# Performance work log

Hardware: AMD Instinct MI355X
Metric: run time of the kernel (lower is better)

## Reference

```python
import jax, jax.numpy as jnp
import numpy as np
from jax import lax

B, C, H, L = 4, 64, 8, 2048  # batch, per-head channels, heads, sequence length


def setup_inputs() -> dict:
    key = jax.random.key(0)
    ks = jax.random.split(key, 15)

    def p(k, shape, s=0.05):
        return jax.random.normal(k, shape, jnp.float32) * s

    inp = {"x": jax.random.normal(ks[0], (B, C, L), jnp.float32)}
    for i, nm in enumerate(["q", "k", "v"]):
        inp[f"{nm}_dw"] = p(ks[1 + 4 * i], (C, 1, 3))       # depthwise conv weight, groups=C, k=3
        inp[f"{nm}_db"] = p(ks[2 + 4 * i], (C,))
        inp[f"{nm}_pw"] = p(ks[3 + 4 * i], (H * C, C))      # pointwise 1x1 conv weight
        inp[f"{nm}_pb"] = p(ks[4 + 4 * i], (H * C,))
    inp["u_w"] = p(ks[13], (C, H * C))                      # unify_heads 1x1 conv weight
    inp["u_b"] = p(ks[14], (C,))
    return inp


def dsconv(x, dw, db, pw, pb):
    # Depth-separable conv1d: depthwise (k=3, pad=1, groups=C) then pointwise 1x1.
    c = x.shape[1]
    y = lax.conv_general_dilated(x, dw, window_strides=(1,), padding=[(1, 1)],
                                 dimension_numbers=("NCH", "OIH", "NCH"),
                                 feature_group_count=c)
    y = y + db[None, :, None]
    return jnp.einsum("bcl,oc->bol", y, pw) + pb[None, :, None]


def reference(x, q_dw, q_db, q_pw, q_pb, k_dw, k_db, k_pw, k_pb,
              v_dw, v_db, v_pw, v_pb, u_w, u_b):
    b, c, l = x.shape
    h = H
    scale = c ** (-0.25)
    q = dsconv(x, q_dw, q_db, q_pw, q_pb).reshape(b, h, c, l) * scale
    k = dsconv(x, k_dw, k_db, k_pw, k_pb).reshape(b, h, c, l) * scale
    v = dsconv(x, v_dw, v_db, v_pw, v_pb).reshape(b, h, c, l)
    # dot[b,h,i,j] = sum_c k[b,h,c,i] * q[b,h,c,j]  (i = key pos, j = query pos)
    dot = jnp.einsum("bhci,bhcj->bhij", k, q)
    att = jax.nn.softmax(dot, axis=2)  # normalize over key positions (torch dim=1 of [bh,l,l])
    out = jnp.einsum("bhci,bhij->bhcj", v, att).reshape(b, h * c, l)
    return jnp.einsum("bkl,ck->bcl", out, u_w) + u_b[None, :, None]
```

## Files before the change

kernel.cpp:

```cpp
#include <hip/hip_runtime.h>
#include <hip/hip_bf16.h>
#include <stdint.h>
#include <string.h>

typedef unsigned short u16;
typedef unsigned int u32;
typedef __bf16 bf16x8 __attribute__((ext_vector_type(8)));
typedef float f32x4 __attribute__((ext_vector_type(4)));
typedef unsigned int u32x2v __attribute__((ext_vector_type(2)));

#define NB 4
#define NC 64
#define NH 8
#define NL 2048
#define HC 512

#define XT_OFF  ((size_t)0)
#define WM_OFF  ((size_t)1 << 20)
#define PBM_OFF ((size_t)2 << 20)
#define V_OFF   ((size_t)4 << 20)
#define QT_OFF  ((size_t)12 << 20)
#define KT_OFF  ((size_t)20 << 20)

#define LP 68

#if __has_builtin(__builtin_amdgcn_exp2f)
#define EXP2F __builtin_amdgcn_exp2f
#else
#define EXP2F exp2f
#endif

static __device__ __forceinline__ u16 f2bfu(float f) {
  union { float f; unsigned int i; } x; x.f = f;
  unsigned int i = x.i;
  return (u16)((i + 0x7fffu + ((i >> 16) & 1u)) >> 16);
}
static __device__ __forceinline__ u32 pk2(float a, float b) {
  float2 f; f.x = a; f.y = b;
  __hip_bfloat162 h = __float22bfloat162_rn(f);
  u32 w; __builtin_memcpy(&w, &h, 4); return w;
}
static __device__ __forceinline__ bf16x8 ld_bf8(const u16* p) {
  bf16x8 v; __builtin_memcpy(&v, p, 16); return v;
}
static __device__ __forceinline__ bf16x8 frag_from4(u32 a, u32 b, u32 c, u32 d) {
  u32 t[4] = {a, b, c, d};
  bf16x8 v; __builtin_memcpy(&v, t, 16); return v;
}
static __device__ __forceinline__ void st_frag(u16* p, u32 a, u32 b, u32 c, u32 d) {
  u32 t[4] = {a, b, c, d};
  __builtin_memcpy(p, t, 16);
}

#define XCHG(X_, Y_, Fa_, Fb_)                                              \
  {                                                                         \
    u32x2v a_ = __builtin_amdgcn_permlane32_swap((X_), (Y_), false, false); \
    u32x2v b_ = __builtin_amdgcn_permlane16_swap(a_.x, a_.y, false, false); \
    Fa_ = b_.x; Fb_ = b_.y;                                                 \
  }

__global__ __launch_bounds__(256) void prep_all(
    const float* __restrict__ x,
    const float* __restrict__ qdw, const float* __restrict__ qdb,
    const float* __restrict__ qpw, const float* __restrict__ qpb,
    const float* __restrict__ kdw, const float* __restrict__ kdb,
    const float* __restrict__ kpw, const float* __restrict__ kpb,
    const float* __restrict__ vdw, const float* __restrict__ vdb,
    const float* __restrict__ vpw, const float* __restrict__ vpb,
    const float* __restrict__ ub,
    u16* __restrict__ Wm, float* __restrict__ pbm,
    u16* __restrict__ xT, float* __restrict__ out)
{
  __shared__ __align__(16) u16 T[64 * LP];
  int bx = blockIdx.x;
  int tid = threadIdx.x;

  if (bx < 512) {
    int i4 = bx * 256 + tid;
    int c = (i4 >> 9) & 63;
    float f = ub[c];
    float4 v = {f, f, f, f};
    ((float4*)out)[i4] = v;
    return;
  }
  if (bx < 902) {
    int idx = (bx - 512) * 256 + tid;
    if (idx < 98304) {
      int tns = idx >> 15, r = idx & 32767, o = r >> 6, c = r & 63;
      const float* dw = (tns == 0) ? qdw : (tns == 1) ? kdw : vdw;
      const float* pw = (tns == 0) ? qpw : (tns == 1) ? kpw : vpw;
      float s = (tns == 0) ? 0.35355339059327373f * 1.4426950408889634f
              : (tns == 1) ? 0.35355339059327373f : 1.0f;
      float w = pw[o * 64 + c] * s;
#pragma unroll
      for (int d = 0; d < 3; ++d)
        Wm[((size_t)(tns * 3 + d) * 512 + o) * 64 + c] = f2bfu(w * dw[c * 3 + d]);
    } else {
      int i = idx - 98304;
      int tns = i >> 9, o = i & 511;
      const float* db = (tns == 0) ? qdb : (tns == 1) ? kdb : vdb;
      const float* pw = (tns == 0) ? qpw : (tns == 1) ? kpw : vpw;
      const float* pb = (tns == 0) ? qpb : (tns == 1) ? kpb : vpb;
      float s = (tns == 0) ? 0.35355339059327373f * 1.4426950408889634f
              : (tns == 1) ? 0.35355339059327373f : 1.0f;
      float bias = pb[o];
      for (int c = 0; c < 64; ++c) bias += pw[o * 64 + c] * db[c];
      pbm[i] = bias * s;
    }
    return;
  }
  {
    int b2 = bx - 902;
    int lt = b2 & 31, b = b2 >> 5;
    {
      int c = tid & 63, ls = (tid >> 6) * 16;
      const float4* g = (const float4*)(x + ((size_t)b * NC + c) * NL + lt * 64 + ls);
      u16 tmp[16];
#pragma unroll
      for (int j4 = 0; j4 < 4; ++j4) {
        float4 f = g[j4];
        tmp[j4*4+0] = f2bfu(f.x); tmp[j4*4+1] = f2bfu(f.y);
        tmp[j4*4+2] = f2bfu(f.z); tmp[j4*4+3] = f2bfu(f.w);
      }
#pragma unroll
      for (int j = 0; j < 16; ++j) T[(ls + j) * LP + c] = tmp[j];
    }
    __syncthreads();
    {
      int r = tid >> 2, cs = (tid & 3) * 16;
      uint4 a = *(const uint4*)&T[r * LP + cs];
      uint4 b3 = *(const uint4*)&T[r * LP + cs + 8];
      u16* o = xT + ((size_t)b * NL + lt * 64 + r) * 64 + cs;
      *(uint4*)o = a;
      *(uint4*)(o + 8) = b3;
    }
  }
}

__global__ __launch_bounds__(256) void qkv_gemm(
    const u16* __restrict__ xT, const u16* __restrict__ Wm,
    const float* __restrict__ pbm,
    u16* __restrict__ v, u16* __restrict__ qT, u16* __restrict__ kT)
{
  __shared__ __align__(16) u16 WS[3][64 * LP];
  __shared__ __align__(16) u16 XS[2][66 * LP];

  int bx = blockIdx.x;
  int lg  = bx & 7;
  int och = (bx >> 3) & 7;
  int tmp = bx >> 6;
  int tns = tmp % 3;
  int b   = tmp / 3;

  int tid = threadIdx.x;
  int wave = tid >> 6, lane = tid & 63, quad = lane >> 4, l16 = lane & 15;
  const u16* xg = xT + (size_t)b * NL * 64;

  {
    const u16* wg = Wm + ((size_t)(tns * 3) * 512 + och * 64) * 64;
#pragma unroll
    for (int it = 0; it < 6; ++it) {
      int s = tid + it * 256;
      int d = s >> 9, r = s & 511;
      int o = r >> 3, c4 = r & 7;
      uint4 w = *(const uint4*)(wg + ((size_t)d * 512 + o) * 64 + c4 * 8);
      *(uint4*)&WS[d][o * LP + c4 * 8] = w;
    }
  }

  int xr0 = tid >> 3,          xc0 = (tid & 7) * 8;
  int xr1 = (tid + 256) >> 3,  xc1 = xc0;
  int xr2 = (tid + 512) >> 3,  xc2 = xc0;
  uint4 R0, R1, R2;
  uint4 Z = {0, 0, 0, 0};

#define LOAD_XS(tt)                                                         \
  {                                                                         \
    int base = (lg * 4 + (tt)) * 64 - 1;                                    \
    int g0 = base + xr0, g1 = base + xr1, g2 = base + xr2;                  \
    R0 = ((unsigned)g0 < NL) ? *(const uint4*)(xg + (size_t)g0 * 64 + xc0) : Z; \
    R1 = ((unsigned)g1 < NL) ? *(const uint4*)(xg + (size_t)g1 * 64 + xc1) : Z; \
    if (tid < 16)                                                           \
      R2 = ((unsigned)g2 < NL) ? *(const uint4*)(xg + (size_t)g2 * 64 + xc2) : Z; \
  }
#define STORE_XS(bf)                                                        \
  {                                                                         \
    *(uint4*)&XS[bf][xr0 * LP + xc0] = R0;                                  \
    *(uint4*)&XS[bf][xr1 * LP + xc1] = R1;                                  \
    if (tid < 16) *(uint4*)&XS[bf][xr2 * LP + xc2] = R2;                    \
  }

  LOAD_XS(0); STORE_XS(0);
  LOAD_XS(1);
  __syncthreads();

  float4 bq4[4];
  float bvv = 0.f;
  bf16x8 aw[3][2];
  if (tns == 2) {
    bvv = pbm[tns * 512 + och * 64 + wave * 16 + l16];
#pragma unroll
    for (int d = 0; d < 3; ++d)
#pragma unroll
      for (int kh = 0; kh < 2; ++kh)
        aw[d][kh] = ld_bf8(&WS[d][(wave * 16 + l16) * LP + kh * 32 + quad * 8]);
  } else {
    const float* pbt = pbm + tns * 512 + och * 64;
#pragma unroll
    for (int nt = 0; nt < 4; ++nt)
      bq4[nt] = *(const float4*)(pbt + nt * 16 + quad * 4);
  }

  for (int t = 0; t < 4; ++t) {
    int cur = t & 1;
    f32x4 acc[4] = {{0,0,0,0},{0,0,0,0},{0,0,0,0},{0,0,0,0}};

    if (tns == 2) {
#pragma unroll
      for (int nt = 0; nt < 4; ++nt)
#pragma unroll
        for (int d = 0; d < 3; ++d)
#pragma unroll
          for (int kh = 0; kh < 2; ++kh) {
            bf16x8 bx8 = ld_bf8(&XS[cur][(nt * 16 + l16 + d) * LP + kh * 32 + quad * 8]);
            acc[nt] = __builtin_amdgcn_mfma_f32_16x16x32_bf16(bx8, aw[d][kh], acc[nt], 0, 0, 0);
          }
    } else {
      bf16x8 ax[3][2];
#pragma unroll
      for (int d = 0; d < 3; ++d)
#pragma unroll
        for (int kh = 0; kh < 2; ++kh)
          ax[d][kh] = ld_bf8(&XS[cur][(wave * 16 + l16 + d) * LP + kh * 32 + quad * 8]);
#pragma unroll
      for (int nt = 0; nt < 4; ++nt)
#pragma unroll
        for (int d = 0; d < 3; ++d)
#pragma unroll
          for (int kh = 0; kh < 2; ++kh) {
            bf16x8 bw = ld_bf8(&WS[d][(nt * 16 + l16) * LP + kh * 32 + quad * 8]);
            acc[nt] = __builtin_amdgcn_mfma_f32_16x16x32_bf16(bw, ax[d][kh], acc[nt], 0, 0, 0);
          }
    }

    if (t < 3) { STORE_XS((t + 1) & 1); if (t < 2) LOAD_XS(t + 2); }
    __syncthreads();

    int lt = lg * 4 + t;
    if (tns == 2) {
      u32 w01[4], w23[4];
#pragma unroll
      for (int nt = 0; nt < 4; ++nt) {
        w01[nt] = pk2(acc[nt][0] + bvv, acc[nt][1] + bvv);
        w23[nt] = pk2(acc[nt][2] + bvv, acc[nt][3] + bvv);
      }
      u16* vp = v + ((size_t)(b * HC + och * 64 + wave * 16 + l16)) * NL + lt * 64;
#pragma unroll
      for (int kh = 0; kh < 2; ++kh) {
        u32 F0, F1, F2, F3;
        XCHG(w01[2 * kh], w01[2 * kh + 1], F0, F2);
        XCHG(w23[2 * kh], w23[2 * kh + 1], F1, F3);
        st_frag(vp + kh * 32 + quad * 8, F0, F1, F2, F3);
      }
    } else {
      u32 w01[4], w23[4];
#pragma unroll
      for (int nt = 0; nt < 4; ++nt) {
        w01[nt] = pk2(acc[nt][0] + bq4[nt].x, acc[nt][1] + bq4[nt].y);
        w23[nt] = pk2(acc[nt][2] + bq4[nt].z, acc[nt][3] + bq4[nt].w);
      }
      u16* dst = (tns == 0) ? qT : kT;
      u16* qp = dst + ((size_t)(b * 8 + och) * NL + lt * 64 + wave * 16 + l16) * 64;
#pragma unroll
      for (int kh = 0; kh < 2; ++kh) {
        u32 F0, F1, F2, F3;
        XCHG(w01[2 * kh], w01[2 * kh + 1], F0, F2);
        XCHG(w23[2 * kh], w23[2 * kh + 1], F1, F3);
        st_frag(qp + kh * 32 + quad * 8, F0, F1, F2, F3);
      }
    }
  }
#undef LOAD_XS
#undef STORE_XS
}

__global__ __launch_bounds__(512, 4) void attn_kernel(
    const u16* __restrict__ qT, const u16* __restrict__ kT,
    const u16* __restrict__ vg, const float* __restrict__ uw,
    float* __restrict__ outg)
{
  __shared__ __align__(16) u16 Kt[2][64 * LP];
  __shared__ __align__(16) u16 Vt[2][64 * LP];
  __shared__ __align__(16) u16 UW[64 * LP];

  int bx = blockIdx.x;
  int qt = bx & 15, bh = bx >> 4;
  int b = bh >> 3, h = bh & 7;
  int tid = threadIdx.x;
  int wave = tid >> 6, lane = tid & 63, quad = lane >> 4, l16 = lane & 15;

  const u16* Qh = qT + (size_t)bh * NL * 64;
  const u16* Kh = kT + (size_t)bh * NL * 64;
  const u16* Vh = vg + ((size_t)(b * HC + h * NC)) * NL;
  int q0 = qt * 128;

  int sr = tid >> 3, ss = (tid & 7) * 8;
  int vc = tid >> 3, vk = (tid & 7) * 8;

  {
    int c = tid >> 3, g = (tid & 7) * 8;
    const float4* s = (const float4*)(uw + (size_t)c * HC + h * 64 + g);
    float4 w0 = s[0], w1 = s[1];
    u16* d = &UW[c * LP + g];
    d[0] = f2bfu(w0.x); d[1] = f2bfu(w0.y); d[2] = f2bfu(w0.z); d[3] = f2bfu(w0.w);
    d[4] = f2bfu(w1.x); d[5] = f2bfu(w1.y); d[6] = f2bfu(w1.z); d[7] = f2bfu(w1.w);
  }

  uint4 ka, va;
  {
    ka = *(const uint4*)(Kh + (size_t)sr * 64 + ss);
    va = *(const uint4*)(Vh + (size_t)vc * NL + vk);
    *(uint4*)&Kt[0][sr * LP + ss] = ka;
    *(uint4*)&Vt[0][vc * LP + vk] = va;
    ka = *(const uint4*)(Kh + (size_t)(64 + sr) * 64 + ss);
    va = *(const uint4*)(Vh + (size_t)vc * NL + 64 + vk);
  }

  bf16x8 bq[2];
#pragma unroll
  for (int kh = 0; kh < 2; ++kh)
    bq[kh] = ld_bf8(Qh + (size_t)(q0 + wave * 16 + l16) * 64 + kh * 32 + quad * 8);

  bf16x8 ones = frag_from4(0x3F803F80u, 0x3F803F80u, 0x3F803F80u, 0x3F803F80u);

  __syncthreads();

  f32x4 o[4];
#pragma unroll
  for (int ct = 0; ct < 4; ++ct) o[ct] = (f32x4){0, 0, 0, 0};
  f32x4 lacc = {0, 0, 0, 0};

  for (int i = 0; i < 32; ++i) {
    int cur = i & 1;
    bf16x8 ak[4][2], av[4][2];
#pragma unroll
    for (int j = 0; j < 4; ++j)
#pragma unroll
      for (int kh = 0; kh < 2; ++kh) {
        ak[j][kh] = ld_bf8(&Kt[cur][(j * 16 + l16) * LP + kh * 32 + quad * 8]);
        av[j][kh] = ld_bf8(&Vt[cur][(j * 16 + l16) * LP + kh * 32 + quad * 8]);
      }

    f32x4 s[4];
#pragma unroll
    for (int ktl = 0; ktl < 4; ++ktl) {
      f32x4 z = {0, 0, 0, 0};
      z = __builtin_amdgcn_mfma_f32_16x16x32_bf16(ak[ktl][0], bq[0], z, 0, 0, 0);
      z = __builtin_amdgcn_mfma_f32_16x16x32_bf16(ak[ktl][1], bq[1], z, 0, 0, 0);
      s[ktl] = z;
    }
    u32 w01[4], w23[4];
#pragma unroll
    for (int ktl = 0; ktl < 4; ++ktl) {
      float p0 = EXP2F(s[ktl][0]);
      float p1 = EXP2F(s[ktl][1]);
      float p2 = EXP2F(s[ktl][2]);
      float p3 = EXP2F(s[ktl][3]);
      w01[ktl] = pk2(p0, p1);
      w23[ktl] = pk2(p2, p3);
    }
#pragma unroll
    for (int kh = 0; kh < 2; ++kh) {
      u32 F0, F1, F2, F3;
      XCHG(w01[2 * kh], w01[2 * kh + 1], F0, F2);
      XCHG(w23[2 * kh], w23[2 * kh + 1], F1, F3);
      bf16x8 bp = frag_from4(F0, F1, F2, F3);
      lacc = __builtin_amdgcn_mfma_f32_16x16x32_bf16(ones, bp, lacc, 0, 0, 0);
#pragma unroll
      for (int ct = 0; ct < 4; ++ct)
        o[ct] = __builtin_amdgcn_mfma_f32_16x16x32_bf16(av[ct][kh], bp, o[ct], 0, 0, 0);
    }

    if (i < 31) {
      int nxt = cur ^ 1;
      *(uint4*)&Kt[nxt][sr * LP + ss] = ka;
      *(uint4*)&Vt[nxt][vc * LP + vk] = va;
      if (i < 30) {
        int kt2 = (i + 2) * 64;
        ka = *(const uint4*)(Kh + (size_t)(kt2 + sr) * 64 + ss);
        va = *(const uint4*)(Vh + (size_t)vc * NL + kt2 + vk);
      }
    }
    __syncthreads();
  }

  float* ob = outg + ((size_t)b * NC) * NL;
  {
    float rinv = 1.0f / lacc[0];

    u32 w01[4], w23[4];
#pragma unroll
    for (int ct = 0; ct < 4; ++ct) {
      w01[ct] = pk2(o[ct][0] * rinv, o[ct][1] * rinv);
      w23[ct] = pk2(o[ct][2] * rinv, o[ct][3] * rinv);
    }
    bf16x8 ot[2];
#pragma unroll
    for (int kh = 0; kh < 2; ++kh) {
      u32 F0, F1, F2, F3;
      XCHG(w01[2 * kh], w01[2 * kh + 1], F0, F2);
      XCHG(w23[2 * kh], w23[2 * kh + 1], F1, F3);
      ot[kh] = frag_from4(F0, F1, F2, F3);
    }

    int qcol = q0 + wave * 16 + l16;
#pragma unroll
    for (int mt = 0; mt < 4; ++mt) {
      f32x4 acc = {0, 0, 0, 0};
#pragma unroll
      for (int kh = 0; kh < 2; ++kh) {
        bf16x8 a = ld_bf8(&UW[(mt * 16 + l16) * LP + kh * 32 + quad * 8]);
        acc = __builtin_amdgcn_mfma_f32_16x16x32_bf16(a, ot[kh], acc, 0, 0, 0);
      }
#pragma unroll
      for (int rr = 0; rr < 4; ++rr) {
        int c = mt * 16 + quad * 4 + rr;
        atomicAdd(&ob[(size_t)c * NL + qcol], acc[rr]);
      }
    }
  }
}

extern "C" void kernel_launch(void* const* d_in, const int* in_sizes, int n_in,
                              void* d_out, int out_size, void* d_ws, size_t ws_size,
                              hipStream_t stream) {
  (void)in_sizes; (void)n_in; (void)out_size; (void)ws_size;
  const float* x   = (const float*)d_in[0];
  const float* qdw = (const float*)d_in[1];
  const float* qdb = (const float*)d_in[2];
  const float* qpw = (const float*)d_in[3];
  const float* qpb = (const float*)d_in[4];
  const float* kdw = (const float*)d_in[5];
  const float* kdb = (const float*)d_in[6];
  const float* kpw = (const float*)d_in[7];
  const float* kpb = (const float*)d_in[8];
  const float* vdw = (const float*)d_in[9];
  const float* vdb = (const float*)d_in[10];
  const float* vpw = (const float*)d_in[11];
  const float* vpb = (const float*)d_in[12];
  const float* uw  = (const float*)d_in[13];
  const float* ub  = (const float*)d_in[14];

  char* ws = (char*)d_ws;
  u16*   xT  = (u16*)(ws + XT_OFF);
  u16*   Wm  = (u16*)(ws + WM_OFF);
  float* pbm = (float*)(ws + PBM_OFF);
  u16*   v   = (u16*)(ws + V_OFF);
  u16*   qT  = (u16*)(ws + QT_OFF);
  u16*   kT  = (u16*)(ws + KT_OFF);
  float* out = (float*)d_out;

  prep_all<<<1030, 256, 0, stream>>>(
      x, qdw, qdb, qpw, qpb, kdw, kdb, kpw, kpb, vdw, vdb, vpw, vpb,
      ub, Wm, pbm, xT, out);
  qkv_gemm<<<768, 256, 0, stream>>>(xT, Wm, pbm, v, qT, kT);
  attn_kernel<<<512, 512, 0, stream>>>(qT, kT, v, uw, out);
}
```

Baseline: 151.7 us.

## Restructure QKV GEMM to one 128-position tile per block with more blocks

Each qkv_gemm block previously looped over four 64-position tiles, double-buffering x through registers and shared memory. Now each block loads a single 130-row x halo tile once, and each wave computes a 32-position by 64-output tile with 8 accumulators, reusing the weight and x fragments across them. The grid doubles to 1536 blocks to add parallelism and remove the serial loop and its barriers. In exchange, the software pipelining between tiles is lost and the weight tile is loaded into shared memory twice as often overall.

```diff
diff --git a/kernel.cpp b/kernel.cpp
--- a/kernel.cpp
+++ b/kernel.cpp
@@ -143,18 +143,20 @@
     u16* __restrict__ v, u16* __restrict__ qT, u16* __restrict__ kT)
 {
   __shared__ __align__(16) u16 WS[3][64 * LP];
-  __shared__ __align__(16) u16 XS[2][66 * LP];
+  __shared__ __align__(16) u16 XS[130 * LP];
 
   int bx = blockIdx.x;
-  int lg  = bx & 7;
-  int och = (bx >> 3) & 7;
-  int tmp = bx >> 6;
+  int lg  = bx & 15;
+  int och = (bx >> 4) & 7;
+  int tmp = bx >> 7;
   int tns = tmp % 3;
   int b   = tmp / 3;
 
   int tid = threadIdx.x;
   int wave = tid >> 6, lane = tid & 63, quad = lane >> 4, l16 = lane & 15;
   const u16* xg = xT + (size_t)b * NL * 64;
+  int L0 = lg * 128;
+  uint4 Z = {0, 0, 0, 0};
 
   {
     const u16* wg = Wm + ((size_t)(tns * 3) * 512 + och * 64) * 64;
@@ -167,110 +169,64 @@
       *(uint4*)&WS[d][o * LP + c4 * 8] = w;
     }
   }
-
-  int xr0 = tid >> 3,          xc0 = (tid & 7) * 8;
-  int xr1 = (tid + 256) >> 3,  xc1 = xc0;
-  int xr2 = (tid + 512) >> 3,  xc2 = xc0;
-  uint4 R0, R1, R2;
-  uint4 Z = {0, 0, 0, 0};
-
-#define LOAD_XS(tt)                                                         \
-  {                                                                         \
-    int base = (lg * 4 + (tt)) * 64 - 1;                                    \
-    int g0 = base + xr0, g1 = base + xr1, g2 = base + xr2;                  \
-    R0 = ((unsigned)g0 < NL) ? *(const uint4*)(xg + (size_t)g0 * 64 + xc0) : Z; \
-    R1 = ((unsigned)g1 < NL) ? *(const uint4*)(xg + (size_t)g1 * 64 + xc1) : Z; \
-    if (tid < 16)                                                           \
-      R2 = ((unsigned)g2 < NL) ? *(const uint4*)(xg + (size_t)g2 * 64 + xc2) : Z; \
-  }
-#define STORE_XS(bf)                                                        \
-  {                                                                         \
-    *(uint4*)&XS[bf][xr0 * LP + xc0] = R0;                                  \
-    *(uint4*)&XS[bf][xr1 * LP + xc1] = R1;                                  \
-    if (tid < 16) *(uint4*)&XS[bf][xr2 * LP + xc2] = R2;                    \
-  }
-
-  LOAD_XS(0); STORE_XS(0);
-  LOAD_XS(1);
+  {
+    int xr = tid >> 3, xc = (tid & 7) * 8;
+#pragma unroll
+    for (int j = 0; j < 4; ++j) {
+      int r = xr + 32 * j;
+      int g = L0 - 1 + r;
+      uint4 w = ((unsigned)g < NL) ? *(const uint4*)(xg + (size_t)g * 64 + xc) : Z;
+      *(uint4*)&XS[r * LP + xc] = w;
+    }
+    if (tid < 16) {
+      int r = 128 + (tid >> 3);
+      int g = L0 - 1 + r;
+      uint4 w = ((unsigned)g < NL) ? *(const uint4*)(xg + (size_t)g * 64 + xc) : Z;
+      *(uint4*)&XS[r * LP + xc] = w;
+    }
+  }
   __syncthreads();
 
-  float4 bq4[4];
-  float bvv = 0.f;
-  bf16x8 aw[3][2];
-  if (tns == 2) {
-    bvv = pbm[tns * 512 + och * 64 + wave * 16 + l16];
-#pragma unroll
-    for (int d = 0; d < 3; ++d)
-#pragma unroll
-      for (int kh = 0; kh < 2; ++kh)
-        aw[d][kh] = ld_bf8(&WS[d][(wave * 16 + l16) * LP + kh * 32 + quad * 8]);
-  } else {
+  f32x4 acc[8] = {{0,0,0,0},{0,0,0,0},{0,0,0,0},{0,0,0,0},
+                  {0,0,0,0},{0,0,0,0},{0,0,0,0},{0,0,0,0}};
+
+  if (tns != 2) {
+    float4 bq4[4];
     const float* pbt = pbm + tns * 512 + och * 64;
 #pragma unroll
     for (int nt = 0; nt < 4; ++nt)
       bq4[nt] = *(const float4*)(pbt + nt * 16 + quad * 4);
-  }
-
-  for (int t = 0; t < 4; ++t) {
-    int cur = t & 1;
-    f32x4 acc[4] = {{0,0,0,0},{0,0,0,0},{0,0,0,0},{0,0,0,0}};
-
-    if (tns == 2) {
-#pragma unroll
-      for (int nt = 0; nt < 4; ++nt)
-#pragma unroll
-        for (int d = 0; d < 3; ++d)
-#pragma unroll
-          for (int kh = 0; kh < 2; ++kh) {
-            bf16x8 bx8 = ld_bf8(&XS[cur][(nt * 16 + l16 + d) * LP + kh * 32 + quad * 8]);
-            acc[nt] = __builtin_amdgcn_mfma_f32_16x16x32_bf16(bx8, aw[d][kh], acc[nt], 0, 0, 0);
-          }
-    } else {
-      bf16x8 ax[3][2];
-#pragma unroll
-      for (int d = 0; d < 3; ++d)
-#pragma unroll
-        for (int kh = 0; kh < 2; ++kh)
-          ax[d][kh] = ld_bf8(&XS[cur][(wave * 16 + l16 + d) * LP + kh * 32 + quad * 8]);
-#pragma unroll
-      for (int nt = 0; nt < 4; ++nt)
-#pragma unroll
-        for (int d = 0; d < 3; ++d)
-#pragma unroll
-          for (int kh = 0; kh < 2; ++kh) {
-            bf16x8 bw = ld_bf8(&WS[d][(nt * 16 + l16) * LP + kh * 32 + quad * 8]);
-            acc[nt] = __builtin_amdgcn_mfma_f32_16x16x32_bf16(bw, ax[d][kh], acc[nt], 0, 0, 0);
-          }
-    }
-
-    if (t < 3) { STORE_XS((t + 1) & 1); if (t < 2) LOAD_XS(t + 2); }
-    __syncthreads();
-
-    int lt = lg * 4 + t;
-    if (tns == 2) {
+
+#pragma unroll
+    for (int d = 0; d < 3; ++d)
+#pragma unroll
+      for (int kh = 0; kh < 2; ++kh) {
+        bf16x8 wf[4], xf[2];
+#pragma unroll
+        for (int nt = 0; nt < 4; ++nt)
+          wf[nt] = ld_bf8(&WS[d][(nt * 16 + l16) * LP + kh * 32 + quad * 8]);
+#pragma unroll
+        for (int lt = 0; lt < 2; ++lt)
+          xf[lt] = ld_bf8(&XS[(wave * 32 + lt * 16 + l16 + d) * LP + kh * 32 + quad * 8]);
+#pragma unroll
+        for (int nt = 0; nt < 4; ++nt)
+#pragma unroll
+          for (int lt = 0; lt < 2; ++lt)
+            acc[nt * 2 + lt] = __builtin_amdgcn_mfma_f32_16x16x32_bf16(
+                wf[nt], xf[lt], acc[nt * 2 + lt], 0, 0, 0);
+      }
+
+    u16* dst = (tns == 0) ? qT : kT;
+#pragma unroll
+    for (int lt = 0; lt < 2; ++lt) {
       u32 w01[4], w23[4];
 #pragma unroll
       for (int nt = 0; nt < 4; ++nt) {
-        w01[nt] = pk2(acc[nt][0] + bvv, acc[nt][1] + bvv);
-        w23[nt] = pk2(acc[nt][2] + bvv, acc[nt][3] + bvv);
-      }
-      u16* vp = v + ((size_t)(b * HC + och * 64 + wave * 16 + l16)) * NL + lt * 64;
-#pragma unroll
-      for (int kh = 0; kh < 2; ++kh) {
-        u32 F0, F1, F2, F3;
-        XCHG(w01[2 * kh], w01[2 * kh + 1], F0, F2);
-        XCHG(w23[2 * kh], w23[2 * kh + 1], F1, F3);
-        st_frag(vp + kh * 32 + quad * 8, F0, F1, F2, F3);
-      }
-    } else {
-      u32 w01[4], w23[4];
-#pragma unroll
-      for (int nt = 0; nt < 4; ++nt) {
-        w01[nt] = pk2(acc[nt][0] + bq4[nt].x, acc[nt][1] + bq4[nt].y);
-        w23[nt] = pk2(acc[nt][2] + bq4[nt].z, acc[nt][3] + bq4[nt].w);
-      }
-      u16* dst = (tns == 0) ? qT : kT;
-      u16* qp = dst + ((size_t)(b * 8 + och) * NL + lt * 64 + wave * 16 + l16) * 64;
+        w01[nt] = pk2(acc[nt * 2 + lt][0] + bq4[nt].x, acc[nt * 2 + lt][1] + bq4[nt].y);
+        w23[nt] = pk2(acc[nt * 2 + lt][2] + bq4[nt].z, acc[nt * 2 + lt][3] + bq4[nt].w);
+      }
+      int l = L0 + wave * 32 + lt * 16 + l16;
+      u16* qp = dst + ((size_t)(b * 8 + och) * NL + l) * 64;
 #pragma unroll
       for (int kh = 0; kh < 2; ++kh) {
         u32 F0, F1, F2, F3;
@@ -279,9 +235,46 @@
         st_frag(qp + kh * 32 + quad * 8, F0, F1, F2, F3);
       }
     }
-  }
-#undef LOAD_XS
-#undef STORE_XS
+  } else {
+    float bv4[4];
+#pragma unroll
+    for (int ot = 0; ot < 4; ++ot)
+      bv4[ot] = pbm[tns * 512 + och * 64 + ot * 16 + l16];
+
+#pragma unroll
+    for (int d = 0; d < 3; ++d)
+#pragma unroll
+      for (int kh = 0; kh < 2; ++kh) {
+        bf16x8 wf[4], xf[2];
+#pragma unroll
+        for (int ot = 0; ot < 4; ++ot)
+          wf[ot] = ld_bf8(&WS[d][(ot * 16 + l16) * LP + kh * 32 + quad * 8]);
+#pragma unroll
+        for (int lt = 0; lt < 2; ++lt)
+          xf[lt] = ld_bf8(&XS[(wave * 32 + lt * 16 + l16 + d) * LP + kh * 32 + quad * 8]);
+#pragma unroll
+        for (int lt = 0; lt < 2; ++lt)
+#pragma unroll
+          for (int ot = 0; ot < 4; ++ot)
+            acc[lt * 4 + ot] = __builtin_amdgcn_mfma_f32_16x16x32_bf16(
+                xf[lt], wf[ot], acc[lt * 4 + ot], 0, 0, 0);
+      }
+
+#pragma unroll
+    for (int ot = 0; ot < 4; ++ot) {
+      u32 a01[2], a23[2];
+#pragma unroll
+      for (int lt = 0; lt < 2; ++lt) {
+        a01[lt] = pk2(acc[lt * 4 + ot][0] + bv4[ot], acc[lt * 4 + ot][1] + bv4[ot]);
+        a23[lt] = pk2(acc[lt * 4 + ot][2] + bv4[ot], acc[lt * 4 + ot][3] + bv4[ot]);
+      }
+      u16* vp = v + ((size_t)(b * HC + och * 64 + ot * 16 + l16)) * NL + L0 + wave * 32;
+      u32 F0, F1, F2, F3;
+      XCHG(a01[0], a01[1], F0, F2);
+      XCHG(a23[0], a23[1], F1, F3);
+      st_frag(vp + quad * 8, F0, F1, F2, F3);
+    }
+  }
 }
 
 __global__ __launch_bounds__(512, 4) void attn_kernel(
@@ -463,6 +456,6 @@
   prep_all<<<1030, 256, 0, stream>>>(
       x, qdw, qdb, qpw, qpb, kdw, kdb, kpw, kpb, vdw, vdb, vpw, vpb,
       ub, Wm, pbm, xT, out);
-  qkv_gemm<<<768, 256, 0, stream>>>(xT, Wm, pbm, v, qT, kT);
+  qkv_gemm<<<1536, 256, 0, stream>>>(xT, Wm, pbm, v, qT, kT);
   attn_kernel<<<512, 512, 0, stream>>>(qT, kT, v, uw, out);
 }
```

New measurement: 153.3 us. Within noise of the previous version (+1.0%).
